# Performance work log

Hardware: AMD Instinct MI355X
Metric: run time of the kernel (lower is better)

The kernel has to match this reference:

```python
import jax, jax.numpy as jnp
import numpy as np
from jax import lax

FEATURE_SIZES = (19, 38, 76)   # 608px YOLOv3 grids
NUM_CLASSES = 80
THR_CONF = 0.5
THR_NMS = 0.3
K = 300                        # max detections kept per image (padded, fixed shape)
EPS = 1e-7


def setup_inputs() -> dict:
    key = jax.random.key(0)
    k1, k2 = jax.random.split(key)
    B = 32
    N = sum(f * f * 3 for f in FEATURE_SIZES)  # 22743
    p_yolo = jax.random.normal(k1, (B, N, 5 + NUM_CLASSES), dtype=jnp.float32)
    # normalized anchor xywh table, kept safely inside (0,1)
    ancs = jax.random.uniform(k2, (N, 4), dtype=jnp.float32, minval=0.05, maxval=0.95)
    # fsize_p = np.repeat(feature_sizes, grid^2*3) as in the torch forward
    fs = np.concatenate([np.full((f * f * 3, 2), f, dtype=np.float32) for f in FEATURE_SIZES], axis=0)
    return {"p_yolo": p_yolo, "ancs": ancs, "fsize_p": jnp.asarray(fs)}


def _iou_matrix(b):
    # b: [K,4] ltrb -> [K,K] pairwise IoU
    area = jnp.maximum(b[:, 2] - b[:, 0], 0.0) * jnp.maximum(b[:, 3] - b[:, 1], 0.0)
    lt = jnp.maximum(b[:, None, :2], b[None, :, :2])
    rb = jnp.minimum(b[:, None, 2:], b[None, :, 2:])
    wh = jnp.maximum(rb - lt, 0.0)
    inter = wh[..., 0] * wh[..., 1]
    return inter / (area[:, None] + area[None, :] - inter + EPS)


def _greedy_nms(iou, valid):
    # iou: [K,K] (rows sorted by descending score), valid: [K] bool
    def body(keep, i):
        suppressed = jnp.any((iou[i] > THR_NMS) & keep)
        k_i = valid[i] & jnp.logical_not(suppressed)
        return keep.at[i].set(k_i), k_i
    keep, _ = lax.scan(body, jnp.zeros(valid.shape[0], dtype=bool), jnp.arange(valid.shape[0]))
    return keep


def reference(p_yolo, ancs, fsize_p):
    # sigmoid_(p[:,:,4:])
    conf = jax.nn.sigmoid(p_yolo[..., 4])          # [B,N]
    cls = jax.nn.sigmoid(p_yolo[..., 5:])          # [B,N,C]
    # fix_boxes4yolo3: xy = sigmoid(txy)/fsize + anc_xy ; wh = exp(twh)*anc_wh
    xy = jax.nn.sigmoid(p_yolo[..., :2]) / fsize_p + ancs[..., :2]
    wh = jnp.exp(p_yolo[..., 2:4]) * ancs[..., 2:]
    ltrb = jnp.concatenate([xy - wh * 0.5, xy + wh * 0.5], axis=-1)  # xywh2ltrb, [B,N,4]
    labels = jnp.argmax(cls, axis=-1) + 1                            # [B,N] int

    valid = conf > THR_CONF
    scores_m = jnp.where(valid, conf, 0.0)
    top_scores, idx = lax.top_k(scores_m, K)                         # [B,K], sorted desc
    boxes_k = jnp.take_along_axis(ltrb, idx[..., None], axis=1)      # [B,K,4]
    labels_k = jnp.take_along_axis(labels, idx, axis=1)              # [B,K]
    valid_k = top_scores > THR_CONF

    # label-aware NMS: offset boxes per class (label_nms semantics); coords live in ~[-1,2]
    boxes_off = boxes_k + labels_k.astype(boxes_k.dtype)[..., None] * 4.0
    iou = jax.vmap(_iou_matrix)(boxes_off)                           # [B,K,K]
    keep = jax.vmap(_greedy_nms)(iou, valid_k)                       # [B,K] bool

    B = p_yolo.shape[0]
    ids_batch = jnp.broadcast_to(jnp.arange(B, dtype=jnp.int32)[:, None], (B, K))
    scores_out = top_scores * keep.astype(top_scores.dtype)          # 0 for suppressed/pad
    labels_out = labels_k * keep.astype(labels_k.dtype)
    return ids_batch, boxes_k, labels_out, scores_out
```

## Files before the change

kernel.cpp:

```cpp
#include <hip/hip_runtime.h>
#include <hip/hip_bf16.h>

#pragma clang fp contract(off)

#define BATCH 32
#define NPOS  22743
#define NPOSP 22744
#define N4P   (NPOSP/4)
#define ROW   85
#define KTOP  300
#define KPAD  512

#define OFF_IDS    0
#define OFF_BOXES  (BATCH*KTOP)
#define OFF_LABELS (OFF_BOXES + BATCH*KTOP*4)
#define OFF_SCORES (OFF_LABELS + BATCH*KTOP)

#define WS_KEYS   0
#define WS_SELIDX (BATCH*NPOSP*4)
#define WS_SELKEY (WS_SELIDX + BATCH*KTOP*4)
#define WS_LABELS (WS_SELKEY + BATCH*KTOP*4)

__device__ __forceinline__ float sigmoidf_ref(float x) {
    return 1.0f / (1.0f + expf(-x));
}

__global__ __launch_bounds__(256) void k_extract(const float* __restrict__ p,
                                                 unsigned* __restrict__ keys) {
    const int n = blockIdx.x * 256 + threadIdx.x;
    const int b = blockIdx.y;
    if (n < NPOS) {
        float x = p[((size_t)b * NPOS + n) * ROW + 4];
        float cf = sigmoidf_ref(x);
        keys[(size_t)b * NPOSP + n] = (cf > 0.5f) ? (__float_as_uint(cf) & 0x00FFFFFFu) : 0u;
    } else if (n < NPOSP) {
        keys[(size_t)b * NPOSP + n] = 0u;
    }
}

__global__ __launch_bounds__(512) void k_select(const unsigned* __restrict__ keys,
                                                int* __restrict__ sel_idx,
                                                unsigned* __restrict__ sel_key) {
    const int b = blockIdx.x;
    const int t = threadIdx.x;
    const int lane = t & 63;
    __shared__ unsigned h[256];
    __shared__ unsigned sc[256];
    __shared__ unsigned bcast_bin, bcast_R;
    __shared__ int cnt, ovf;
    __shared__ unsigned long long arr[KPAD];
    const unsigned* kb = keys + (size_t)b * NPOSP;
    const uint4* kb4 = reinterpret_cast<const uint4*>(kb);

    unsigned prefix = 0;
    unsigned R = KTOP;

    for (int pass = 0; pass < 3; ++pass) {
        const int shift = 16 - 8 * pass;
        if (t < 256) h[t] = 0;
        __syncthreads();
        int zc = 0;
        for (int i4 = t; i4 < N4P; i4 += 512) {
            uint4 u4 = kb4[i4];
            unsigned uu[4] = {u4.x, u4.y, u4.z, u4.w};
            #pragma unroll
            for (int c = 0; c < 4; ++c) {
                unsigned u = uu[c];
                bool match = (pass == 0) || ((u >> (shift + 8)) == prefix);
                if (match) {
                    if (u) atomicAdd(&h[(u >> shift) & 255], 1u);
                    else   ++zc;
                }
            }
        }
        #pragma unroll
        for (int d = 32; d; d >>= 1) zc += __shfl_xor(zc, d);
        if (lane == 0 && zc) atomicAdd(&h[0], (unsigned)zc);
        __syncthreads();
        if (t < 256) sc[t] = h[t];
        __syncthreads();
        for (int off = 1; off < 256; off <<= 1) {
            unsigned add = (t < 256 && t + off < 256) ? sc[t + off] : 0u;
            __syncthreads();
            if (t < 256) sc[t] += add;
            __syncthreads();
        }
        if (t < 256) {
            unsigned snext = (t < 255) ? sc[t + 1] : 0u;
            if (sc[t] >= R && snext < R) { bcast_bin = (unsigned)t; bcast_R = R - snext; }
        }
        __syncthreads();
        prefix = (prefix << 8) | bcast_bin;
        R = bcast_R;
        __syncthreads();
    }
    const unsigned T = prefix;

    if (t == 0) { cnt = 0; ovf = 0; }
    for (int e = t; e < KPAD; e += 512) arr[e] = 0ull;
    __syncthreads();
    for (int i4 = t; i4 < N4P; i4 += 512) {
        uint4 u4 = kb4[i4];
        unsigned uu[4] = {u4.x, u4.y, u4.z, u4.w};
        #pragma unroll
        for (int c = 0; c < 4; ++c) {
            unsigned u = uu[c];
            if (u >= T) {
                int n = i4 * 4 + c;
                int pos = atomicAdd(&cnt, 1);
                if (pos < KPAD) arr[pos] = ((unsigned long long)u << 32) | (unsigned)(~n);
                else ovf = 1;
            }
        }
    }
    __syncthreads();
    if (ovf) {
        if (t == 0) cnt = 0;
        __syncthreads();
        for (int e = t; e < KPAD; e += 512) arr[e] = 0ull;
        __syncthreads();
        for (int n = t; n < NPOS; n += 512) {
            unsigned u = kb[n];
            if (u > T) {
                int pos = atomicAdd(&cnt, 1);
                if (pos < KPAD) arr[pos] = ((unsigned long long)u << 32) | (unsigned)(~n);
            }
        }
        __syncthreads();
        if (t == 0) {
            int c = min(cnt, KPAD - 1);
            for (int n = 0; n < NPOS && c < KTOP; ++n)
                if (kb[n] == T) arr[c++] = ((unsigned long long)T << 32) | (unsigned)(~n);
        }
        __syncthreads();
    }
    for (unsigned kk = 2; kk <= KPAD; kk <<= 1)
        for (unsigned j = kk >> 1; j > 0; j >>= 1) {
            __syncthreads();
            unsigned e = (unsigned)t, partner = e ^ j;
            if (partner > e) {
                bool up = ((e & kk) == 0);
                unsigned long long a = arr[e], bb = arr[partner];
                if (up ? (a > bb) : (a < bb)) { arr[e] = bb; arr[partner] = a; }
            }
        }
    __syncthreads();
    if (t < KTOP) {
        unsigned long long v = arr[KPAD - 1 - t];
        sel_idx[b * KTOP + t] = (int)(~(unsigned)v);
        sel_key[b * KTOP + t] = (unsigned)(v >> 32);
    }
}

__global__ __launch_bounds__(256) void k_decode(const float* __restrict__ p,
                                                const float* __restrict__ ancs,
                                                const float* __restrict__ fsz,
                                                const int* __restrict__ sel_idx,
                                                int* __restrict__ labels,
                                                float* __restrict__ out) {
    const int wid = (int)((blockIdx.x * blockDim.x + threadIdx.x) >> 6);
    const int lane = threadIdx.x & 63;
    if (wid >= BATCH * KTOP) return;
    const int b = wid / KTOP, k = wid % KTOP;
    const int n = sel_idx[b * KTOP + k];
    const size_t base = ((size_t)b * NPOS + n) * ROW;

    float v1 = p[base + lane];
    float v2 = (lane < 21) ? p[base + 64 + lane] : -INFINITY;

    float bv = -INFINITY; int bc = 1 << 20;
    if (lane >= 5) { bv = v1; bc = lane - 5; }
    if (lane < 21) {
        int c2 = 59 + lane;
        if (v2 > bv || (v2 == bv && c2 < bc)) { bv = v2; bc = c2; }
    }
    for (int d = 32; d; d >>= 1) {
        float ov = __shfl_xor(bv, d);
        int   oc = __shfl_xor(bc, d);
        if (ov > bv || (ov == bv && oc < bc)) { bv = ov; bc = oc; }
    }
    const int label = bc + 1;

    float t0 = __shfl(v1, 0), t1 = __shfl(v1, 1), t2 = __shfl(v1, 2), t3 = __shfl(v1, 3);
    if (lane == 0) {
        float f0 = fsz[(size_t)n * 2 + 0], f1 = fsz[(size_t)n * 2 + 1];
        float a0 = ancs[(size_t)n * 4 + 0], a1 = ancs[(size_t)n * 4 + 1];
        float a2 = ancs[(size_t)n * 4 + 2], a3 = ancs[(size_t)n * 4 + 3];
        float cx = sigmoidf_ref(t0) / f0 + a0;
        float cy = sigmoidf_ref(t1) / f1 + a1;
        float w  = expf(t2) * a2;
        float hh = expf(t3) * a3;
        float* ob = out + OFF_BOXES + (size_t)(b * KTOP + k) * 4;
        ob[0] = cx - w * 0.5f;
        ob[1] = cy - hh * 0.5f;
        ob[2] = cx + w * 0.5f;
        ob[3] = cy + hh * 0.5f;
        out[OFF_IDS + b * KTOP + k] = (float)b;
        labels[b * KTOP + k] = label;
    }
}

__global__ __launch_bounds__(512) void k_nms(const float* __restrict__ boxes,
                                             const int* __restrict__ labels,
                                             const unsigned* __restrict__ sel_key,
                                             float* __restrict__ out) {
    const int b = blockIdx.x, t = threadIdx.x;
    const int lane = t & 63, wave = t >> 6;
    __shared__ float4 bx4[KTOP];
    __shared__ float  area_s[KTOP];
    __shared__ float  score_s[KTOP];
    __shared__ int    lab_s[KTOP];
    __shared__ unsigned long long O[KTOP * 5];
    __shared__ unsigned long long vb[5];
    __shared__ unsigned long long kw[5];

    bool valid = false;
    if (t < KTOP) {
        const float* p4 = boxes + (size_t)(b * KTOP + t) * 4;
        int L = labels[b * KTOP + t];
        float off = (float)L * 4.0f;
        float l = p4[0] + off, tp = p4[1] + off, r = p4[2] + off, bt = p4[3] + off;
        bx4[t] = make_float4(l, tp, r, bt);
        area_s[t] = fmaxf(r - l, 0.0f) * fmaxf(bt - tp, 0.0f);
        lab_s[t] = L;
        unsigned key = sel_key[b * KTOP + t];
        valid = (key != 0u);
        score_s[t] = __uint_as_float(key | 0x3F000000u);
    }
    unsigned long long vbw = __ballot(valid);
    if (lane == 0 && wave < 5) vb[wave] = vbw;
    __syncthreads();

    for (int i = wave; i < KTOP; i += 8) {
        float4 bi = bx4[i];
        float  ai = area_s[i];
        int qmax = (i + 63) >> 6;
        for (int q = 0; q < 5; ++q) {
            unsigned long long w = 0ull;
            if (q < qmax) {
                int j = q * 64 + lane;
                bool pred = false;
                if (j < i) {
                    float4 bj = bx4[j];
                    float lt0 = fmaxf(bi.x, bj.x);
                    float lt1 = fmaxf(bi.y, bj.y);
                    float rb0 = fminf(bi.z, bj.z);
                    float rb1 = fminf(bi.w, bj.w);
                    float ww = fmaxf(rb0 - lt0, 0.0f);
                    float hh = fmaxf(rb1 - lt1, 0.0f);
                    float inter = ww * hh;
                    float iou = inter / (((ai + area_s[j]) - inter) + 1e-7f);
                    pred = iou > 0.3f;
                }
                w = __ballot(pred);
            }
            if (lane == 0) O[i * 5 + q] = w;
        }
    }
    __syncthreads();

    if (t < 64) {
        unsigned long long kwl = 0ull;
        unsigned long long vbl = (lane < 5) ? vb[lane] : 0ull;
        unsigned long long cur = (lane < 5) ? O[lane] : 0ull;
        for (int i = 0; i < KTOP; ++i) {
            unsigned long long nxt = (lane < 5 && i < KTOP - 1) ? O[(i + 1) * 5 + lane] : 0ull;
            bool sup = __any((cur & kwl) != 0ull);
            if (lane == (i >> 6)) {
                bool v = (vbl >> (i & 63)) & 1ull;
                if (v && !sup) kwl |= 1ull << (i & 63);
            }
            cur = nxt;
        }
        if (lane < 5) kw[lane] = kwl;
    }
    __syncthreads();

    if (t < KTOP) {
        bool kp = (kw[t >> 6] >> (t & 63)) & 1ull;
        out[OFF_SCORES + b * KTOP + t] = kp ? score_s[t] : 0.0f;
        out[OFF_LABELS + b * KTOP + t] = kp ? (float)lab_s[t] : 0.0f;
    }
}

extern "C" void kernel_launch(void* const* d_in, const int* in_sizes, int n_in,
                              void* d_out, int out_size, void* d_ws, size_t ws_size,
                              hipStream_t stream) {
    const float* p    = (const float*)d_in[0];
    const float* ancs = (const float*)d_in[1];
    const float* fsz  = (const float*)d_in[2];
    float* out = (float*)d_out;

    char* w = (char*)d_ws;
    unsigned* keys    = (unsigned*)(w + WS_KEYS);
    int*      sel_idx = (int*)(w + WS_SELIDX);
    unsigned* sel_key = (unsigned*)(w + WS_SELKEY);
    int*      labels  = (int*)(w + WS_LABELS);

    hipLaunchKernelGGL(k_extract, dim3((NPOSP + 255) / 256, BATCH), dim3(256), 0, stream, p, keys);
    hipLaunchKernelGGL(k_select, dim3(BATCH), dim3(512), 0, stream, keys, sel_idx, sel_key);
    hipLaunchKernelGGL(k_decode, dim3((BATCH * KTOP + 3) / 4), dim3(256), 0, stream,
                       p, ancs, fsz, sel_idx, labels, out);
    hipLaunchKernelGGL(k_nms, dim3(BATCH), dim3(512), 0, stream, out + OFF_BOXES, labels, sel_key, out);
}
```

Before: 385.2 us.

## Replace three-pass radix select with single 1024-bin histogram pass and fallback

The top-K selection now builds one 1024-bin histogram over the top 11 bits of the 24-bit confidence key and picks a coarse threshold bin. Every key at or above that bin is gathered into the 512-slot buffer and then sorted. This replaces three histogram passes over the keys with one histogram pass plus one gather pass. If more than 512 candidates pass the coarse threshold, the code falls back to the original exact three-pass radix select.

```diff
diff --git a/kernel.cpp b/kernel.cpp
--- a/kernel.cpp
+++ b/kernel.cpp
@@ -10,6 +10,7 @@
 #define ROW   85
 #define KTOP  300
 #define KPAD  512
+#define NBIN  1024
 
 #define OFF_IDS    0
 #define OFF_BOXES  (BATCH*KTOP)
@@ -44,21 +45,18 @@
     const int b = blockIdx.x;
     const int t = threadIdx.x;
     const int lane = t & 63;
-    __shared__ unsigned h[256];
-    __shared__ unsigned sc[256];
-    __shared__ unsigned bcast_bin, bcast_R;
+    __shared__ unsigned h[NBIN];
+    __shared__ unsigned s512[512];
+    __shared__ unsigned bcast_bin, bcast_G;
     __shared__ int cnt, ovf;
     __shared__ unsigned long long arr[KPAD];
     const unsigned* kb = keys + (size_t)b * NPOSP;
     const uint4* kb4 = reinterpret_cast<const uint4*>(kb);
 
-    unsigned prefix = 0;
-    unsigned R = KTOP;
-
-    for (int pass = 0; pass < 3; ++pass) {
-        const int shift = 16 - 8 * pass;
-        if (t < 256) h[t] = 0;
-        __syncthreads();
+    h[t] = 0;
+    if (t < NBIN - 512) h[t + 512] = 0;
+    __syncthreads();
+    {
         int zc = 0;
         for (int i4 = t; i4 < N4P; i4 += 512) {
             uint4 u4 = kb4[i4];
@@ -66,62 +64,103 @@
             #pragma unroll
             for (int c = 0; c < 4; ++c) {
                 unsigned u = uu[c];
+                if (u) atomicAdd(&h[u >> 13], 1u);
+                else   ++zc;
+            }
+        }
+        #pragma unroll
+        for (int d = 32; d; d >>= 1) zc += __shfl_xor(zc, d);
+        if (lane == 0 && zc) atomicAdd(&h[0], (unsigned)zc);
+    }
+    __syncthreads();
+    unsigned c0 = h[2 * t], c1 = h[2 * t + 1];
+    s512[t] = c0 + c1;
+    __syncthreads();
+    for (int off = 1; off < 512; off <<= 1) {
+        unsigned add = (t + off < 512) ? s512[t + off] : 0u;
+        __syncthreads();
+        s512[t] += add;
+        __syncthreads();
+    }
+    {
+        unsigned S = s512[t];
+        unsigned Snext = (t < 511) ? s512[t + 1] : 0u;
+        if (S >= KTOP && Snext < KTOP) {
+            unsigned s1 = c1 + Snext;
+            if (s1 >= KTOP) { bcast_bin = 2u * t + 1u; bcast_G = Snext; }
+            else            { bcast_bin = 2u * t;      bcast_G = s1; }
+        }
+    }
+    __syncthreads();
+    const unsigned B = bcast_bin;
+
+    bool fast_ok = false;
+    if (B > 0) {
+        const unsigned T = B << 13;
+        if (t == 0) { cnt = 0; ovf = 0; }
+        arr[t] = 0ull;
+        __syncthreads();
+        for (int i4 = t; i4 < N4P; i4 += 512) {
+            uint4 u4 = kb4[i4];
+            unsigned uu[4] = {u4.x, u4.y, u4.z, u4.w};
+            #pragma unroll
+            for (int c = 0; c < 4; ++c) {
+                unsigned u = uu[c];
+                if (u >= T) {
+                    int n = i4 * 4 + c;
+                    int pos = atomicAdd(&cnt, 1);
+                    if (pos < KPAD) arr[pos] = ((unsigned long long)u << 32) | (unsigned)(~n);
+                    else ovf = 1;
+                }
+            }
+        }
+        __syncthreads();
+        fast_ok = (ovf == 0);
+    }
+
+    if (!fast_ok) {
+        unsigned prefix = 0, R = KTOP;
+        for (int pass = 0; pass < 3; ++pass) {
+            const int shift = 16 - 8 * pass;
+            if (t < 256) h[t] = 0;
+            __syncthreads();
+            int zc2 = 0;
+            for (int n = t; n < NPOSP; n += 512) {
+                unsigned u = kb[n];
                 bool match = (pass == 0) || ((u >> (shift + 8)) == prefix);
                 if (match) {
                     if (u) atomicAdd(&h[(u >> shift) & 255], 1u);
-                    else   ++zc;
+                    else   ++zc2;
                 }
             }
-        }
-        #pragma unroll
-        for (int d = 32; d; d >>= 1) zc += __shfl_xor(zc, d);
-        if (lane == 0 && zc) atomicAdd(&h[0], (unsigned)zc);
-        __syncthreads();
-        if (t < 256) sc[t] = h[t];
-        __syncthreads();
-        for (int off = 1; off < 256; off <<= 1) {
-            unsigned add = (t < 256 && t + off < 256) ? sc[t + off] : 0u;
-            __syncthreads();
-            if (t < 256) sc[t] += add;
-            __syncthreads();
-        }
-        if (t < 256) {
-            unsigned snext = (t < 255) ? sc[t + 1] : 0u;
-            if (sc[t] >= R && snext < R) { bcast_bin = (unsigned)t; bcast_R = R - snext; }
-        }
-        __syncthreads();
-        prefix = (prefix << 8) | bcast_bin;
-        R = bcast_R;
-        __syncthreads();
-    }
-    const unsigned T = prefix;
-
-    if (t == 0) { cnt = 0; ovf = 0; }
-    for (int e = t; e < KPAD; e += 512) arr[e] = 0ull;
-    __syncthreads();
-    for (int i4 = t; i4 < N4P; i4 += 512) {
-        uint4 u4 = kb4[i4];
-        unsigned uu[4] = {u4.x, u4.y, u4.z, u4.w};
-        #pragma unroll
-        for (int c = 0; c < 4; ++c) {
-            unsigned u = uu[c];
-            if (u >= T) {
-                int n = i4 * 4 + c;
-                int pos = atomicAdd(&cnt, 1);
-                if (pos < KPAD) arr[pos] = ((unsigned long long)u << 32) | (unsigned)(~n);
-                else ovf = 1;
-            }
-        }
-    }
-    __syncthreads();
-    if (ovf) {
+            #pragma unroll
+            for (int d = 32; d; d >>= 1) zc2 += __shfl_xor(zc2, d);
+            if (lane == 0 && zc2) atomicAdd(&h[0], (unsigned)zc2);
+            __syncthreads();
+            if (t < 256) s512[t] = h[t];
+            __syncthreads();
+            for (int off = 1; off < 256; off <<= 1) {
+                unsigned add = (t < 256 && t + off < 256) ? s512[t + off] : 0u;
+                __syncthreads();
+                if (t < 256) s512[t] += add;
+                __syncthreads();
+            }
+            if (t < 256) {
+                unsigned snext = (t < 255) ? s512[t + 1] : 0u;
+                if (s512[t] >= R && snext < R) { bcast_bin = (unsigned)t; bcast_G = R - snext; }
+            }
+            __syncthreads();
+            prefix = (prefix << 8) | bcast_bin;
+            R = bcast_G;
+            __syncthreads();
+        }
+        const unsigned Tex = prefix;
         if (t == 0) cnt = 0;
-        __syncthreads();
-        for (int e = t; e < KPAD; e += 512) arr[e] = 0ull;
+        arr[t] = 0ull;
         __syncthreads();
         for (int n = t; n < NPOS; n += 512) {
             unsigned u = kb[n];
-            if (u > T) {
+            if (u > Tex) {
                 int pos = atomicAdd(&cnt, 1);
                 if (pos < KPAD) arr[pos] = ((unsigned long long)u << 32) | (unsigned)(~n);
             }
@@ -130,10 +169,11 @@
         if (t == 0) {
             int c = min(cnt, KPAD - 1);
             for (int n = 0; n < NPOS && c < KTOP; ++n)
-                if (kb[n] == T) arr[c++] = ((unsigned long long)T << 32) | (unsigned)(~n);
-        }
-        __syncthreads();
-    }
+                if (kb[n] == Tex) arr[c++] = ((unsigned long long)Tex << 32) | (unsigned)(~n);
+        }
+        __syncthreads();
+    }
+
     for (unsigned kk = 2; kk <= KPAD; kk <<= 1)
         for (unsigned j = kk >> 1; j > 0; j >>= 1) {
             __syncthreads();
```

Result: no change. 378.1 us (-1.9%).
